# Optimization experiments

Measured on AMD Instinct MI355X. Metric: run time of the kernel, lower is better.

## Reference

```python
import jax, jax.numpy as jnp
import numpy as np

NC = 80        # number of classes
CONF = 0.25    # confidence threshold
RATIO = 0.1    # top-k fraction


def setup_inputs() -> dict:
    key = jax.random.key(0)
    N = 2097152
    data = jax.random.normal(key, (1, N, 4 + NC), dtype=jnp.float32)
    return {"data": data}


def reference(data):
    pred = data[0]                      # [N, 4+nc]
    cls_logits = pred[:, -NC:]          # [N, nc]
    boxes = pred[:, :4]                 # [N, 4]
    scores = jnp.max(cls_logits, axis=1)  # class_id is None -> max over classes
    n = scores.shape[0]
    k = max(1, min(n, int(np.ceil(n * float(RATIO)))))  # static k
    vals, idx = jax.lax.top_k(scores, k)   # [k], [k]
    mask = vals >= CONF                     # [k] bool
    # torch returns 0.0 when mask is empty; masked sums naturally give 0 then.
    loss = jnp.sum(jnp.where(mask, vals, 0.0))
    # output_type == 'all' -> add gathered box sums for masked top-k indices
    loss = loss + jnp.sum(jnp.where(mask[:, None], boxes[idx], 0.0))
    return loss
```

## Files before the change

### kernel.cpp

```cpp
#include <hip/hip_runtime.h>
#include <stdint.h>
#include <math.h>

#define ROWLEN 84
#define F4PR 21
#define RPB 256
#define F4PT (RPB * F4PR)
#define TIECAP 16384u

__device__ __forceinline__ uint32_t map_f(float f) {
    uint32_t u = __float_as_uint(f);
    return (u & 0x80000000u) ? ~u : (u | 0x80000000u);
}
__device__ __forceinline__ float unmap_f(uint32_t u) {
    uint32_t b = (u & 0x80000000u) ? (u & 0x7FFFFFFFu) : ~u;
    return __uint_as_float(b);
}

__device__ void find_parallel(const uint32_t* __restrict__ hist, int nbins, uint32_t target,
                              uint32_t* s, uint32_t* sc2, uint32_t* outBin, uint32_t* outAbove) {
    int tid = threadIdx.x;
    int chunks = nbins / 256;
    int base = tid * chunks;
    uint32_t part = 0;
    for (int i = 0; i < chunks; ++i) part += hist[base + i];
    s[tid] = part;
    __syncthreads();
    for (int off = 1; off < 256; off <<= 1) {
        uint32_t v = (tid + off < 256) ? s[tid + off] : 0u;
        __syncthreads();
        s[tid] += v;
        __syncthreads();
    }
    uint32_t above_next = (tid < 255) ? s[tid + 1] : 0u;
    bool mine = (s[tid] >= target) && (above_next < target);
    if (mine) { sc2[0] = (uint32_t)tid; sc2[1] = above_next; }
    __syncthreads();
    uint32_t c = sc2[0], above = sc2[1];
    if (tid == 0) {
        uint32_t acc = above;
        int b = (int)c * chunks + chunks - 1;
        for (;; --b) {
            uint32_t hb = hist[b];
            if (acc + hb >= target) break;
            acc += hb;
        }
        sc2[0] = (uint32_t)b;
        sc2[1] = acc;
    }
    __syncthreads();
    *outBin = sc2[0];
    *outAbove = sc2[1];
}

__global__ __launch_bounds__(256) void k_score_hist(const float* __restrict__ pred,
                                                    uint32_t* __restrict__ scores,
                                                    uint32_t* __restrict__ gH1,
                                                    uint32_t* __restrict__ ticket, int n) {
    __shared__ float pm[F4PT];
    __shared__ uint32_t h[1024];
    __shared__ int s_tile;
    int tid = threadIdx.x;
    for (int i = tid; i < 1024; i += 256) h[i] = 0;
    uint32_t tid21 = (uint32_t)tid % 21u;
    const float4* pf4 = (const float4*)pred;
    size_t total_f4 = (size_t)n * F4PR;
    int ntiles = (n + RPB - 1) / RPB;
    for (;;) {
        __syncthreads();
        if (tid == 0) s_tile = (int)atomicAdd(ticket, 1u);
        __syncthreads();
        int tile = s_tile;
        if (tile >= ntiles) break;
        size_t gbase = (size_t)tile * F4PT;
        int row0 = tile * RPB;
        if (row0 + RPB <= n) {
#pragma unroll
            for (int it = 0; it < F4PR; ++it) {
                const uint32_t BP = (21u - (4u * (uint32_t)it) % 21u) % 21u;
                float4 v = pf4[gbase + it * 256 + tid];
                float m = fmaxf(fmaxf(v.x, v.y), fmaxf(v.z, v.w));
                pm[it * 256 + tid] = (tid21 == BP) ? -INFINITY : m;
            }
        } else {
#pragma unroll
            for (int it = 0; it < F4PR; ++it) {
                const uint32_t BP = (21u - (4u * (uint32_t)it) % 21u) % 21u;
                int l = it * 256 + tid;
                size_t g = gbase + l;
                float m = -INFINITY;
                if (g < total_f4 && tid21 != BP) {
                    float4 v = pf4[g];
                    m = fmaxf(fmaxf(v.x, v.y), fmaxf(v.z, v.w));
                }
                pm[l] = m;
            }
        }
        __syncthreads();
        int row = row0 + tid;
        if (row < n) {
            const float* q = pm + tid * F4PR;
            float m = q[1];
#pragma unroll
            for (int j = 2; j <= 20; ++j) m = fmaxf(m, q[j]);
            uint32_t u = map_f(m);
            scores[row] = u;
            atomicAdd(&h[u >> 22], 1u);
        }
    }
    __syncthreads();
    for (int i = tid; i < 1024; i += 256)
        if (h[i]) atomicAdd(&gH1[i], h[i]);
}

__global__ void k_sel1(const uint32_t* __restrict__ gH1, uint32_t* __restrict__ sres, uint32_t K) {
    __shared__ uint32_t s[256];
    __shared__ uint32_t sc2[2];
    uint32_t bin, above;
    find_parallel(gH1, 1024, K, s, sc2, &bin, &above);
    if (threadIdx.x == 0) { sres[0] = bin; sres[1] = above; }
}

__global__ void k_hist2(const uint32_t* __restrict__ scores, const uint32_t* __restrict__ sres,
                        uint32_t* __restrict__ gH2, int n) {
    __shared__ uint32_t h[2048];
    for (int i = threadIdx.x; i < 2048; i += blockDim.x) h[i] = 0;
    __syncthreads();
    uint32_t bin1 = sres[0];
    int stride = gridDim.x * blockDim.x;
    for (int r = blockIdx.x * blockDim.x + threadIdx.x; r < n; r += stride) {
        uint32_t u = scores[r];
        if ((u >> 22) == bin1) atomicAdd(&h[(u >> 11) & 0x7FFu], 1u);
    }
    __syncthreads();
    for (int i = threadIdx.x; i < 2048; i += blockDim.x)
        if (h[i]) atomicAdd(&gH2[i], h[i]);
}

__global__ void k_sel2(const uint32_t* __restrict__ gH2, uint32_t* __restrict__ sres, uint32_t K) {
    __shared__ uint32_t s[256];
    __shared__ uint32_t sc2[2];
    uint32_t chi1 = sres[1];
    uint32_t bin, above;
    find_parallel(gH2, 2048, K - chi1, s, sc2, &bin, &above);
    if (threadIdx.x == 0) { sres[2] = bin; sres[3] = above; }
}

__global__ void k_hist3(const uint32_t* __restrict__ scores, const uint32_t* __restrict__ sres,
                        uint32_t* __restrict__ gH3, int n) {
    __shared__ uint32_t h[2048];
    for (int i = threadIdx.x; i < 2048; i += blockDim.x) h[i] = 0;
    __syncthreads();
    uint32_t pref = (sres[0] << 11) | sres[2];
    int stride = gridDim.x * blockDim.x;
    for (int r = blockIdx.x * blockDim.x + threadIdx.x; r < n; r += stride) {
        uint32_t u = scores[r];
        if ((u >> 11) == pref) atomicAdd(&h[u & 0x7FFu], 1u);
    }
    __syncthreads();
    for (int i = threadIdx.x; i < 2048; i += blockDim.x)
        if (h[i]) atomicAdd(&gH3[i], h[i]);
}

__global__ void k_sel3(const uint32_t* __restrict__ gH3, uint32_t* __restrict__ sres, uint32_t K) {
    __shared__ uint32_t s[256];
    __shared__ uint32_t sc2[2];
    uint32_t chi1 = sres[1], chi2 = sres[3];
    uint32_t bin, above;
    find_parallel(gH3, 2048, K - chi1 - chi2, s, sc2, &bin, &above);
    if (threadIdx.x == 0) {
        uint32_t t_u = (sres[0] << 22) | (sres[2] << 11) | bin;
        uint32_t C_gt = chi1 + chi2 + above;
        sres[4] = bin;
        sres[5] = above;
        sres[6] = t_u;
        sres[7] = K - C_gt;
    }
}

__global__ void k_select(const float* __restrict__ pred, const uint32_t* __restrict__ scores,
                         const uint32_t* __restrict__ sres,
                         uint32_t* __restrict__ tieCnt, uint32_t* __restrict__ tieBuf,
                         float* __restrict__ out, int n) {
    __shared__ float wsum[4];
    uint32_t t_u = sres[6];
    const uint32_t u_conf = 0xBE800000u;
    bool tcut = (t_u >= u_conf);
    float lsum = 0.f;
    int stride = gridDim.x * blockDim.x;
    for (int r = blockIdx.x * blockDim.x + threadIdx.x; r < n; r += stride) {
        uint32_t u = scores[r];
        bool sel = tcut ? (u > t_u) : (u >= u_conf);
        if (sel) {
            float4 b = *(const float4*)(pred + (size_t)r * ROWLEN);
            lsum += unmap_f(u) + b.x + b.y + b.z + b.w;
        }
        if (tcut && u == t_u) {
            uint32_t pos = atomicAdd(tieCnt, 1u);
            if (pos < TIECAP) tieBuf[pos] = (uint32_t)r;
        }
    }
    for (int off = 32; off; off >>= 1) lsum += __shfl_down(lsum, off);
    int wid = threadIdx.x >> 6, lane = threadIdx.x & 63;
    if (lane == 0) wsum[wid] = lsum;
    __syncthreads();
    if (threadIdx.x == 0) atomicAdd(out, wsum[0] + wsum[1] + wsum[2] + wsum[3]);
}

__global__ void k_ties(const float* __restrict__ pred, const uint32_t* __restrict__ sres,
                       const uint32_t* __restrict__ tieCnt, const uint32_t* __restrict__ tieBuf,
                       float* __restrict__ out) {
    __shared__ float wsum[4];
    uint32_t t_u = sres[6];
    const uint32_t u_conf = 0xBE800000u;
    if (t_u < u_conf) return;
    uint32_t m = sres[7];
    uint32_t cnt = *tieCnt;
    if (cnt > TIECAP) cnt = TIECAP;
    float lsum = 0.f;
    if (m >= cnt) {
        for (uint32_t i = threadIdx.x; i < cnt; i += blockDim.x) {
            uint32_t r = tieBuf[i];
            float4 b = *(const float4*)(pred + (size_t)r * ROWLEN);
            lsum += b.x + b.y + b.z + b.w;
        }
    } else {
        for (uint32_t i = threadIdx.x; i < cnt; i += blockDim.x) {
            uint32_t ri = tieBuf[i];
            uint32_t rank = 0;
            for (uint32_t j = 0; j < cnt; ++j) rank += (tieBuf[j] < ri) ? 1u : 0u;
            if (rank < m) {
                float4 b = *(const float4*)(pred + (size_t)ri * ROWLEN);
                lsum += b.x + b.y + b.z + b.w;
            }
        }
    }
    for (int off = 32; off; off >>= 1) lsum += __shfl_down(lsum, off);
    int wid = threadIdx.x >> 6, lane = threadIdx.x & 63;
    if (lane == 0) wsum[wid] = lsum;
    __syncthreads();
    if (threadIdx.x == 0)
        atomicAdd(out, wsum[0] + wsum[1] + wsum[2] + wsum[3] + (float)m * unmap_f(t_u));
}

extern "C" void kernel_launch(void* const* d_in, const int* in_sizes, int n_in,
                              void* d_out, int out_size, void* d_ws, size_t ws_size,
                              hipStream_t stream) {
    const float* pred = (const float*)d_in[0];
    int n = in_sizes[0] / ROWLEN;
    double kd = ceil((double)n * 0.1);
    long kk = (long)kd;
    if (kk < 1) kk = 1;
    if (kk > n) kk = n;
    uint32_t K = (uint32_t)kk;

    uint32_t* ws32 = (uint32_t*)d_ws;
    uint32_t* scores = ws32;
    uint32_t* gH1 = ws32 + n;
    uint32_t* gH2 = gH1 + 1024;
    uint32_t* gH3 = gH2 + 2048;
    uint32_t* sres = gH3 + 2048;
    uint32_t* tieCnt = sres + 16;
    uint32_t* ticket = tieCnt + 16;
    uint32_t* tieBuf = ticket + 16;

    hipMemsetAsync(d_out, 0, sizeof(float), stream);
    hipMemsetAsync(gH1, 0, (1024 + 2048 + 2048 + 16 + 16 + 16) * sizeof(uint32_t), stream);

    k_score_hist<<<2048, 256, 0, stream>>>(pred, scores, gH1, ticket, n);
    k_sel1<<<1, 256, 0, stream>>>(gH1, sres, K);
    k_hist2<<<1024, 256, 0, stream>>>(scores, sres, gH2, n);
    k_sel2<<<1, 256, 0, stream>>>(gH2, sres, K);
    k_hist3<<<1024, 256, 0, stream>>>(scores, sres, gH3, n);
    k_sel3<<<1, 256, 0, stream>>>(gH3, sres, K);
    k_select<<<2048, 256, 0, stream>>>(pred, scores, sres, tieCnt, tieBuf, (float*)d_out, n);
    k_ties<<<1, 256, 0, stream>>>(pred, sres, tieCnt, tieBuf, (float*)d_out);
}
```

Before: 236.1 us.

## Fuse radix-select pipeline into single cooperative persistent kernel with grid syncs

Replaces the chain of memsets and eight kernel launches (score/histogram, three select passes, selection, tie handling) with one cooperative kernel that runs all phases separated by grid.sync. Every block recomputes the bin search from the global histogram, so the single-block select kernels go away. This removes launch gaps and tail effects between stages. In exchange it adds grid-wide barrier costs, caps the grid at occupancy×CU (at most 1024 blocks) for the streaming phases, and serializes the tie pass behind a grid sync. The old multi-kernel path is kept as a fallback if the cooperative launch fails.

```diff
diff --git a/kernel.cpp b/kernel.cpp
--- a/kernel.cpp
+++ b/kernel.cpp
@@ -1,4 +1,5 @@
 #include <hip/hip_runtime.h>
+#include <hip/hip_cooperative_groups.h>
 #include <stdint.h>
 #include <math.h>
 
@@ -7,6 +8,8 @@
 #define RPB 256
 #define F4PT (RPB * F4PR)
 #define TIECAP 16384u
+
+namespace cg = cooperative_groups;
 
 __device__ __forceinline__ uint32_t map_f(float f) {
     uint32_t u = __float_as_uint(f);
@@ -52,6 +55,177 @@
     *outBin = sc2[0];
     *outAbove = sc2[1];
 }
+
+
+struct SMem {
+    union {
+        struct { float pm[F4PT]; uint32_t h[1024]; } p1;
+        struct { uint32_t h[2048]; uint32_t s[256]; uint32_t sc2[2]; float wsum[4]; } p2;
+    } u;
+    int s_tile;
+};
+
+__global__ __launch_bounds__(256, 4) void k_fused(const float* __restrict__ pred,
+                                                  uint32_t* __restrict__ scores,
+                                                  uint32_t* __restrict__ gH1,
+                                                  uint32_t* __restrict__ gH2,
+                                                  uint32_t* __restrict__ gH3,
+                                                  uint32_t* __restrict__ tieCnt,
+                                                  uint32_t* __restrict__ ticket,
+                                                  uint32_t* __restrict__ tieBuf,
+                                                  float* __restrict__ out,
+                                                  int n, uint32_t K) {
+    cg::grid_group grid = cg::this_grid();
+    __shared__ SMem sm;
+    int tid = threadIdx.x;
+    int gid = blockIdx.x * 256 + tid;
+    int gstride = gridDim.x * 256;
+
+    for (int i = gid; i < 1024; i += gstride) gH1[i] = 0;
+    for (int i = gid; i < 2048; i += gstride) { gH2[i] = 0; gH3[i] = 0; }
+    if (gid == 0) { *tieCnt = 0; *ticket = 0; *out = 0.f; }
+    grid.sync();
+
+    for (int i = tid; i < 1024; i += 256) sm.u.p1.h[i] = 0;
+    uint32_t tid21 = (uint32_t)tid % 21u;
+    const float4* pf4 = (const float4*)pred;
+    size_t total_f4 = (size_t)n * F4PR;
+    int ntiles = (n + RPB - 1) / RPB;
+    for (;;) {
+        __syncthreads();
+        if (tid == 0) sm.s_tile = (int)atomicAdd(ticket, 1u);
+        __syncthreads();
+        int tile = sm.s_tile;
+        if (tile >= ntiles) break;
+        size_t gbase = (size_t)tile * F4PT;
+        int row0 = tile * RPB;
+        if (row0 + RPB <= n) {
+#pragma unroll
+            for (int it = 0; it < F4PR; ++it) {
+                const uint32_t BP = (21u - (4u * (uint32_t)it) % 21u) % 21u;
+                float4 v = pf4[gbase + it * 256 + tid];
+                float m = fmaxf(fmaxf(v.x, v.y), fmaxf(v.z, v.w));
+                sm.u.p1.pm[it * 256 + tid] = (tid21 == BP) ? -INFINITY : m;
+            }
+        } else {
+#pragma unroll
+            for (int it = 0; it < F4PR; ++it) {
+                const uint32_t BP = (21u - (4u * (uint32_t)it) % 21u) % 21u;
+                int l = it * 256 + tid;
+                size_t g = gbase + l;
+                float m = -INFINITY;
+                if (g < total_f4 && tid21 != BP) {
+                    float4 v = pf4[g];
+                    m = fmaxf(fmaxf(v.x, v.y), fmaxf(v.z, v.w));
+                }
+                sm.u.p1.pm[l] = m;
+            }
+        }
+        __syncthreads();
+        int row = row0 + tid;
+        if (row < n) {
+            const float* q = sm.u.p1.pm + tid * F4PR;
+            float m = q[1];
+#pragma unroll
+            for (int j = 2; j <= 20; ++j) m = fmaxf(m, q[j]);
+            uint32_t u = map_f(m);
+            scores[row] = u;
+            atomicAdd(&sm.u.p1.h[u >> 22], 1u);
+        }
+    }
+    __syncthreads();
+    for (int i = tid; i < 1024; i += 256) {
+        uint32_t hv = sm.u.p1.h[i];
+        if (hv) atomicAdd(&gH1[i], hv);
+    }
+    grid.sync();
+
+    for (int i = tid; i < 2048; i += 256) sm.u.p2.h[i] = 0;
+    uint32_t bin1, chi1;
+    find_parallel(gH1, 1024, K, sm.u.p2.s, sm.u.p2.sc2, &bin1, &chi1);
+    for (int r = gid; r < n; r += gstride) {
+        uint32_t u = scores[r];
+        if ((u >> 22) == bin1) atomicAdd(&sm.u.p2.h[(u >> 11) & 0x7FFu], 1u);
+    }
+    __syncthreads();
+    for (int i = tid; i < 2048; i += 256) {
+        uint32_t hv = sm.u.p2.h[i];
+        if (hv) atomicAdd(&gH2[i], hv);
+    }
+    grid.sync();
+
+    for (int i = tid; i < 2048; i += 256) sm.u.p2.h[i] = 0;
+    uint32_t bin2, chi2;
+    find_parallel(gH2, 2048, K - chi1, sm.u.p2.s, sm.u.p2.sc2, &bin2, &chi2);
+    uint32_t pref = (bin1 << 11) | bin2;
+    for (int r = gid; r < n; r += gstride) {
+        uint32_t u = scores[r];
+        if ((u >> 11) == pref) atomicAdd(&sm.u.p2.h[u & 0x7FFu], 1u);
+    }
+    __syncthreads();
+    for (int i = tid; i < 2048; i += 256) {
+        uint32_t hv = sm.u.p2.h[i];
+        if (hv) atomicAdd(&gH3[i], hv);
+    }
+    grid.sync();
+
+    uint32_t bin3, chi3;
+    find_parallel(gH3, 2048, K - chi1 - chi2, sm.u.p2.s, sm.u.p2.sc2, &bin3, &chi3);
+    uint32_t t_u = (bin1 << 22) | (bin2 << 11) | bin3;
+    uint32_t m_ties = K - (chi1 + chi2 + chi3);
+    const uint32_t u_conf = 0xBE800000u;
+    bool tcut = (t_u >= u_conf);
+    float lsum = 0.f;
+    for (int r = gid; r < n; r += gstride) {
+        uint32_t u = scores[r];
+        bool sel = tcut ? (u > t_u) : (u >= u_conf);
+        if (sel) {
+            float4 b = *(const float4*)(pred + (size_t)r * ROWLEN);
+            lsum += unmap_f(u) + b.x + b.y + b.z + b.w;
+        }
+        if (tcut && u == t_u) {
+            uint32_t pos = atomicAdd(tieCnt, 1u);
+            if (pos < TIECAP) tieBuf[pos] = (uint32_t)r;
+        }
+    }
+    for (int off = 32; off; off >>= 1) lsum += __shfl_down(lsum, off);
+    int wid = tid >> 6, lane = tid & 63;
+    if (lane == 0) sm.u.p2.wsum[wid] = lsum;
+    __syncthreads();
+    if (tid == 0)
+        atomicAdd(out, sm.u.p2.wsum[0] + sm.u.p2.wsum[1] + sm.u.p2.wsum[2] + sm.u.p2.wsum[3]);
+    grid.sync();
+
+    if (blockIdx.x == 0 && tcut) {
+        uint32_t cnt = *tieCnt;
+        if (cnt > TIECAP) cnt = TIECAP;
+        float tsum = 0.f;
+        if (m_ties >= cnt) {
+            for (uint32_t i = tid; i < cnt; i += 256) {
+                uint32_t r = tieBuf[i];
+                float4 b = *(const float4*)(pred + (size_t)r * ROWLEN);
+                tsum += b.x + b.y + b.z + b.w;
+            }
+        } else {
+            for (uint32_t i = tid; i < cnt; i += 256) {
+                uint32_t ri = tieBuf[i];
+                uint32_t rank = 0;
+                for (uint32_t j = 0; j < cnt; ++j) rank += (tieBuf[j] < ri) ? 1u : 0u;
+                if (rank < m_ties) {
+                    float4 b = *(const float4*)(pred + (size_t)ri * ROWLEN);
+                    tsum += b.x + b.y + b.z + b.w;
+                }
+            }
+        }
+        for (int off = 32; off; off >>= 1) tsum += __shfl_down(tsum, off);
+        if (lane == 0) sm.u.p2.wsum[wid] = tsum;
+        __syncthreads();
+        if (tid == 0)
+            atomicAdd(out, sm.u.p2.wsum[0] + sm.u.p2.wsum[1] + sm.u.p2.wsum[2] + sm.u.p2.wsum[3]
+                           + (float)m_ties * unmap_f(t_u));
+    }
+}
+
 
 __global__ __launch_bounds__(256) void k_score_hist(const float* __restrict__ pred,
                                                     uint32_t* __restrict__ scores,
@@ -243,6 +417,7 @@
         atomicAdd(out, wsum[0] + wsum[1] + wsum[2] + wsum[3] + (float)m * unmap_f(t_u));
 }
 
+
 extern "C" void kernel_launch(void* const* d_in, const int* in_sizes, int n_in,
                               void* d_out, int out_size, void* d_ws, size_t ws_size,
                               hipStream_t stream) {
@@ -263,16 +438,40 @@
     uint32_t* tieCnt = sres + 16;
     uint32_t* ticket = tieCnt + 16;
     uint32_t* tieBuf = ticket + 16;
-
-    hipMemsetAsync(d_out, 0, sizeof(float), stream);
-    hipMemsetAsync(gH1, 0, (1024 + 2048 + 2048 + 16 + 16 + 16) * sizeof(uint32_t), stream);
-
-    k_score_hist<<<2048, 256, 0, stream>>>(pred, scores, gH1, ticket, n);
-    k_sel1<<<1, 256, 0, stream>>>(gH1, sres, K);
-    k_hist2<<<1024, 256, 0, stream>>>(scores, sres, gH2, n);
-    k_sel2<<<1, 256, 0, stream>>>(gH2, sres, K);
-    k_hist3<<<1024, 256, 0, stream>>>(scores, sres, gH3, n);
-    k_sel3<<<1, 256, 0, stream>>>(gH3, sres, K);
-    k_select<<<2048, 256, 0, stream>>>(pred, scores, sres, tieCnt, tieBuf, (float*)d_out, n);
-    k_ties<<<1, 256, 0, stream>>>(pred, sres, tieCnt, tieBuf, (float*)d_out);
-}
+    float* out = (float*)d_out;
+
+    int dev = 0;
+    (void)hipGetDevice(&dev);
+    int nCU = 0;
+    (void)hipDeviceGetAttribute(&nCU, hipDeviceAttributeMultiprocessorCount, dev);
+    int blkPerCU = 0;
+    hipError_t qe = hipOccupancyMaxActiveBlocksPerMultiprocessor(&blkPerCU, k_fused, 256, 0);
+
+    bool coop_ok = false;
+    if (qe == hipSuccess && nCU > 0 && blkPerCU > 0) {
+        int grid = blkPerCU * nCU;
+        if (grid > 1024) grid = 1024;
+        if (grid >= 64) {
+            void* args[] = {(void*)&pred, (void*)&scores, (void*)&gH1, (void*)&gH2, (void*)&gH3,
+                            (void*)&tieCnt, (void*)&ticket, (void*)&tieBuf, (void*)&out,
+                            (void*)&n, (void*)&K};
+            hipError_t le = hipLaunchCooperativeKernel((void*)k_fused, dim3(grid), dim3(256),
+                                                       args, 0, stream);
+            if (le == hipSuccess) coop_ok = true;
+            else (void)hipGetLastError();
+        }
+    }
+
+    if (!coop_ok) {
+        hipMemsetAsync(d_out, 0, sizeof(float), stream);
+        hipMemsetAsync(gH1, 0, (1024 + 2048 + 2048 + 16 + 16 + 16) * sizeof(uint32_t), stream);
+        k_score_hist<<<2048, 256, 0, stream>>>(pred, scores, gH1, ticket, n);
+        k_sel1<<<1, 256, 0, stream>>>(gH1, sres, K);
+        k_hist2<<<1024, 256, 0, stream>>>(scores, sres, gH2, n);
+        k_sel2<<<1, 256, 0, stream>>>(gH2, sres, K);
+        k_hist3<<<1024, 256, 0, stream>>>(scores, sres, gH3, n);
+        k_sel3<<<1, 256, 0, stream>>>(gH3, sres, K);
+        k_select<<<2048, 256, 0, stream>>>(pred, scores, sres, tieCnt, tieBuf, out, n);
+        k_ties<<<1, 256, 0, stream>>>(pred, sres, tieCnt, tieBuf, out);
+    }
+}
```

Measured after the change: 449.0 us. +90.1%, slower.

## Fuse radix-select bin search into histogram kernels and drop dynamic tile tickets

Applied to the files above, without the earlier changes.

Each single-block selection kernel (sel1/sel2/sel3) is folded into the following histogram or select kernel: every block redundantly scans the previous global histogram to find its bin, and block 0 records the result. The atomic ticket scheduler in the score kernel is replaced with a static grid-stride tile loop, and the output memset is replaced by block 0 zeroing the output. This removes three tiny launches and one memset, trading them for redundant per-block histogram scans and a static work split.

```diff
diff --git a/kernel.cpp b/kernel.cpp
--- a/kernel.cpp
+++ b/kernel.cpp
@@ -56,22 +56,18 @@
 __global__ __launch_bounds__(256) void k_score_hist(const float* __restrict__ pred,
                                                     uint32_t* __restrict__ scores,
                                                     uint32_t* __restrict__ gH1,
-                                                    uint32_t* __restrict__ ticket, int n) {
+                                                    float* __restrict__ out, int n) {
     __shared__ float pm[F4PT];
     __shared__ uint32_t h[1024];
-    __shared__ int s_tile;
     int tid = threadIdx.x;
+    if (blockIdx.x == 0 && tid == 0) *out = 0.f;
     for (int i = tid; i < 1024; i += 256) h[i] = 0;
     uint32_t tid21 = (uint32_t)tid % 21u;
     const float4* pf4 = (const float4*)pred;
     size_t total_f4 = (size_t)n * F4PR;
     int ntiles = (n + RPB - 1) / RPB;
-    for (;;) {
-        __syncthreads();
-        if (tid == 0) s_tile = (int)atomicAdd(ticket, 1u);
-        __syncthreads();
-        int tile = s_tile;
-        if (tile >= ntiles) break;
+    for (int tile = blockIdx.x; tile < ntiles; tile += gridDim.x) {
+        __syncthreads();
         size_t gbase = (size_t)tile * F4PT;
         int row0 = tile * RPB;
         if (row0 + RPB <= n) {
@@ -113,82 +109,67 @@
         if (h[i]) atomicAdd(&gH1[i], h[i]);
 }
 
-__global__ void k_sel1(const uint32_t* __restrict__ gH1, uint32_t* __restrict__ sres, uint32_t K) {
+__global__ void k_hist2f(const uint32_t* __restrict__ scores, const uint32_t* __restrict__ gH1,
+                         uint32_t* __restrict__ gH2, uint32_t* __restrict__ sres,
+                         int n, uint32_t K) {
+    __shared__ uint32_t h[2048];
     __shared__ uint32_t s[256];
     __shared__ uint32_t sc2[2];
-    uint32_t bin, above;
-    find_parallel(gH1, 1024, K, s, sc2, &bin, &above);
-    if (threadIdx.x == 0) { sres[0] = bin; sres[1] = above; }
-}
-
-__global__ void k_hist2(const uint32_t* __restrict__ scores, const uint32_t* __restrict__ sres,
-                        uint32_t* __restrict__ gH2, int n) {
-    __shared__ uint32_t h[2048];
-    for (int i = threadIdx.x; i < 2048; i += blockDim.x) h[i] = 0;
-    __syncthreads();
-    uint32_t bin1 = sres[0];
-    int stride = gridDim.x * blockDim.x;
-    for (int r = blockIdx.x * blockDim.x + threadIdx.x; r < n; r += stride) {
+    for (int i = threadIdx.x; i < 2048; i += 256) h[i] = 0;
+    uint32_t bin1, chi1;
+    find_parallel(gH1, 1024, K, s, sc2, &bin1, &chi1);
+    if (blockIdx.x == 0 && threadIdx.x == 0) { sres[0] = bin1; sres[1] = chi1; }
+    int stride = gridDim.x * 256;
+    for (int r = blockIdx.x * 256 + threadIdx.x; r < n; r += stride) {
         uint32_t u = scores[r];
         if ((u >> 22) == bin1) atomicAdd(&h[(u >> 11) & 0x7FFu], 1u);
     }
     __syncthreads();
-    for (int i = threadIdx.x; i < 2048; i += blockDim.x)
+    for (int i = threadIdx.x; i < 2048; i += 256)
         if (h[i]) atomicAdd(&gH2[i], h[i]);
 }
 
-__global__ void k_sel2(const uint32_t* __restrict__ gH2, uint32_t* __restrict__ sres, uint32_t K) {
+__global__ void k_hist3f(const uint32_t* __restrict__ scores, const uint32_t* __restrict__ gH2,
+                         uint32_t* __restrict__ gH3, uint32_t* __restrict__ sres,
+                         int n, uint32_t K) {
+    __shared__ uint32_t h[2048];
     __shared__ uint32_t s[256];
     __shared__ uint32_t sc2[2];
-    uint32_t chi1 = sres[1];
-    uint32_t bin, above;
-    find_parallel(gH2, 2048, K - chi1, s, sc2, &bin, &above);
-    if (threadIdx.x == 0) { sres[2] = bin; sres[3] = above; }
-}
-
-__global__ void k_hist3(const uint32_t* __restrict__ scores, const uint32_t* __restrict__ sres,
-                        uint32_t* __restrict__ gH3, int n) {
-    __shared__ uint32_t h[2048];
-    for (int i = threadIdx.x; i < 2048; i += blockDim.x) h[i] = 0;
-    __syncthreads();
-    uint32_t pref = (sres[0] << 11) | sres[2];
-    int stride = gridDim.x * blockDim.x;
-    for (int r = blockIdx.x * blockDim.x + threadIdx.x; r < n; r += stride) {
+    for (int i = threadIdx.x; i < 2048; i += 256) h[i] = 0;
+    uint32_t bin1 = sres[0], chi1 = sres[1];
+    uint32_t bin2, chi2;
+    find_parallel(gH2, 2048, K - chi1, s, sc2, &bin2, &chi2);
+    if (blockIdx.x == 0 && threadIdx.x == 0) { sres[2] = bin2; sres[3] = chi2; }
+    uint32_t pref = (bin1 << 11) | bin2;
+    int stride = gridDim.x * 256;
+    for (int r = blockIdx.x * 256 + threadIdx.x; r < n; r += stride) {
         uint32_t u = scores[r];
         if ((u >> 11) == pref) atomicAdd(&h[u & 0x7FFu], 1u);
     }
     __syncthreads();
-    for (int i = threadIdx.x; i < 2048; i += blockDim.x)
+    for (int i = threadIdx.x; i < 2048; i += 256)
         if (h[i]) atomicAdd(&gH3[i], h[i]);
 }
 
-__global__ void k_sel3(const uint32_t* __restrict__ gH3, uint32_t* __restrict__ sres, uint32_t K) {
+__global__ void k_selectf(const float* __restrict__ pred, const uint32_t* __restrict__ scores,
+                          const uint32_t* __restrict__ gH3, uint32_t* __restrict__ sres,
+                          uint32_t* __restrict__ tieCnt, uint32_t* __restrict__ tieBuf,
+                          float* __restrict__ out, int n, uint32_t K) {
     __shared__ uint32_t s[256];
     __shared__ uint32_t sc2[2];
-    uint32_t chi1 = sres[1], chi2 = sres[3];
-    uint32_t bin, above;
-    find_parallel(gH3, 2048, K - chi1 - chi2, s, sc2, &bin, &above);
-    if (threadIdx.x == 0) {
-        uint32_t t_u = (sres[0] << 22) | (sres[2] << 11) | bin;
-        uint32_t C_gt = chi1 + chi2 + above;
-        sres[4] = bin;
-        sres[5] = above;
-        sres[6] = t_u;
-        sres[7] = K - C_gt;
-    }
-}
-
-__global__ void k_select(const float* __restrict__ pred, const uint32_t* __restrict__ scores,
-                         const uint32_t* __restrict__ sres,
-                         uint32_t* __restrict__ tieCnt, uint32_t* __restrict__ tieBuf,
-                         float* __restrict__ out, int n) {
     __shared__ float wsum[4];
-    uint32_t t_u = sres[6];
+    uint32_t bin1 = sres[0], chi1 = sres[1];
+    uint32_t bin2 = sres[2], chi2 = sres[3];
+    uint32_t bin3, chi3;
+    find_parallel(gH3, 2048, K - chi1 - chi2, s, sc2, &bin3, &chi3);
+    uint32_t t_u = (bin1 << 22) | (bin2 << 11) | bin3;
+    uint32_t m_ties = K - (chi1 + chi2 + chi3);
+    if (blockIdx.x == 0 && threadIdx.x == 0) { sres[6] = t_u; sres[7] = m_ties; }
     const uint32_t u_conf = 0xBE800000u;
     bool tcut = (t_u >= u_conf);
     float lsum = 0.f;
-    int stride = gridDim.x * blockDim.x;
-    for (int r = blockIdx.x * blockDim.x + threadIdx.x; r < n; r += stride) {
+    int stride = gridDim.x * 256;
+    for (int r = blockIdx.x * 256 + threadIdx.x; r < n; r += stride) {
         uint32_t u = scores[r];
         bool sel = tcut ? (u > t_u) : (u >= u_conf);
         if (sel) {
@@ -259,20 +240,16 @@
     uint32_t* gH1 = ws32 + n;
     uint32_t* gH2 = gH1 + 1024;
     uint32_t* gH3 = gH2 + 2048;
-    uint32_t* sres = gH3 + 2048;
-    uint32_t* tieCnt = sres + 16;
-    uint32_t* ticket = tieCnt + 16;
-    uint32_t* tieBuf = ticket + 16;
-
-    hipMemsetAsync(d_out, 0, sizeof(float), stream);
-    hipMemsetAsync(gH1, 0, (1024 + 2048 + 2048 + 16 + 16 + 16) * sizeof(uint32_t), stream);
-
-    k_score_hist<<<2048, 256, 0, stream>>>(pred, scores, gH1, ticket, n);
-    k_sel1<<<1, 256, 0, stream>>>(gH1, sres, K);
-    k_hist2<<<1024, 256, 0, stream>>>(scores, sres, gH2, n);
-    k_sel2<<<1, 256, 0, stream>>>(gH2, sres, K);
-    k_hist3<<<1024, 256, 0, stream>>>(scores, sres, gH3, n);
-    k_sel3<<<1, 256, 0, stream>>>(gH3, sres, K);
-    k_select<<<2048, 256, 0, stream>>>(pred, scores, sres, tieCnt, tieBuf, (float*)d_out, n);
-    k_ties<<<1, 256, 0, stream>>>(pred, sres, tieCnt, tieBuf, (float*)d_out);
-}
+    uint32_t* tieCnt = gH3 + 2048;
+    uint32_t* sres = tieCnt + 16;
+    uint32_t* tieBuf = sres + 16;
+    float* out = (float*)d_out;
+
+    hipMemsetAsync(gH1, 0, (1024 + 2048 + 2048 + 16) * sizeof(uint32_t), stream);
+
+    k_score_hist<<<2048, 256, 0, stream>>>(pred, scores, gH1, out, n);
+    k_hist2f<<<1024, 256, 0, stream>>>(scores, gH1, gH2, sres, n, K);
+    k_hist3f<<<1024, 256, 0, stream>>>(scores, gH2, gH3, sres, n, K);
+    k_selectf<<<2048, 256, 0, stream>>>(pred, scores, gH3, sres, tieCnt, tieBuf, out, n, K);
+    k_ties<<<1, 256, 0, stream>>>(pred, sres, tieCnt, tieBuf, out);
+}
```

Measured after the change: 201.3 us. 14.8% less time.
